# Optimization experiments

Measured on AMD Instinct MI355X. Metric: run time of the kernel, lower is better.

Reference implementation:

```python
import jax, jax.numpy as jnp
import numpy as np

LOSS_IDX = jnp.array([0, 1])    # loss_indices from __init__
BASIS_IDX = jnp.array([0, 1])   # dtw_mapping_basis (x, y)


def _dtw_path(cost):
    """Classic DTW DP + backtrack on cost [N, M].
    Returns padded alignment path (a, b) of length N+M-1 with validity mask.
    DP is run as an anti-diagonal wavefront scan (L = N+M-1 steps)."""
    N, M = cost.shape
    L = N + M - 1
    inf = jnp.float32(jnp.inf)
    i_idx = jnp.arange(N)

    def diag_step(carry, k):
        prev1, prev2 = carry  # diagonals k-1 and k-2, indexed by row i
        j = k - i_idx
        valid = (j >= 0) & (j < M)
        c = cost[i_idx, jnp.clip(j, 0, M - 1)]
        up = jnp.concatenate([jnp.full((1,), inf), prev1[:-1]])  # D[i-1, j]
        dg = jnp.concatenate([jnp.full((1,), inf), prev2[:-1]])  # D[i-1, j-1]
        lf = prev1                                               # D[i, j-1]
        best = jnp.minimum(jnp.minimum(up, dg), lf)
        best = jnp.where(jnp.isinf(best), jnp.float32(0.0), best)  # (0,0) seed
        cur = jnp.where(valid, c + best, inf)
        return (cur, prev1), cur

    init = (jnp.full((N,), inf), jnp.full((N,), inf))
    _, diags = jax.lax.scan(diag_step, init, jnp.arange(L))  # [L, N]: D[i,j] = diags[i+j, i]

    def getD(i, j):
        ok = (i >= 0) & (j >= 0)
        return jnp.where(ok, diags[jnp.clip(i + j, 0, L - 1), jnp.clip(i, 0, N - 1)], inf)

    def bt_step(carry, _):
        i, j, done = carry
        emit_valid = jnp.logical_not(done)
        cand = jnp.stack([getD(i - 1, j - 1), getD(i - 1, j), getD(i, j - 1)])
        m = jnp.argmin(cand)  # 0: diag, 1: up, 2: left
        ni = jnp.where(m == 2, i, i - 1)
        nj = jnp.where(m == 1, j, j - 1)
        done2 = done | ((i == 0) & (j == 0))
        ni = jnp.where(done2, 0, ni)
        nj = jnp.where(done2, 0, nj)
        return (ni, nj, done2), (i, j, emit_valid)

    init_bt = (jnp.int32(N - 1), jnp.int32(M - 1), jnp.bool_(False))
    _, (a, b, valid) = jax.lax.scan(bt_step, init_bt, None, length=L)
    return a, b, valid


def _dtw_loss_single(pred, targ, subcoef):
    # DTW alignment is computed on detached (numpy in torch) basis coords.
    p = jax.lax.stop_gradient(pred)[:, BASIS_IDX]
    t = jax.lax.stop_gradient(targ)[:, BASIS_IDX]
    # euclidean pairwise distance cost [N, M]
    cost = jnp.sqrt(jnp.sum((p[:, None, :] - t[None, :, :]) ** 2, axis=-1))
    a, b, valid = _dtw_path(cost)
    d = jnp.abs(pred[a][:, LOSS_IDX] - targ[b][:, LOSS_IDX]) * subcoef  # [L, 2]
    return jnp.sum(d * valid[:, None].astype(d.dtype))


def setup_inputs() -> dict:
    key = jax.random.key(0)
    k1, k2 = jax.random.split(key)
    B, N, M, F = 32, 1024, 1024, 4
    preds = jax.random.normal(k1, (B, N, F), dtype=jnp.float32)
    targs = jax.random.normal(k2, (B, M, F), dtype=jnp.float32)
    subcoef = jnp.ones((2,), dtype=jnp.float32)
    return {"preds": preds, "targs": targs, "subcoef": subcoef}


def reference(preds, targs, subcoef):
    per_sample = jax.vmap(_dtw_loss_single, in_axes=(0, 0, None))(preds, targs, subcoef)
    return jnp.sum(per_sample)
```

## Files before the change

kernel.cpp:

```cpp
#include <hip/hip_runtime.h>
#include <math.h>

#define BATCH 32
#define NN 1024
#define MM 1024
#define LPATH (NN + MM - 1)

#define PB 128
#define PQ 128
#define GB 8
#define GH 8
#define PAN_WORDS 1536
#define BAT_WORDS (GB * GH * PAN_WORDS)
#define RCPL (9 * 1024)
#define RC_OFFW ((size_t)BATCH * BAT_WORDS)
#define BR_OFFW (RC_OFFW + (size_t)BATCH * RCPL)
#define WS_WORDS (BR_OFFW + (size_t)BATCH * RCPL)
#define REQ_WS_NEW (WS_WORDS * 4)

#define DEC_WORDS_PER_BATCH ((NN / 4) * (MM / 4))
#define REQ_WS ((size_t)BATCH * DEC_WORDS_PER_BATCH * 4)

__global__ void init_kernel(float* out) { out[0] = 0.0f; }

__global__ void init2(float* __restrict__ ws, float* __restrict__ out)
{
    const int b = blockIdx.x, t = threadIdx.x;
    const float INF = __builtin_inff();
    if (b == 0 && t == 0) out[0] = 0.0f;
    float* rc0 = ws + RC_OFFW + (size_t)b * RCPL;
    float* br0 = ws + BR_OFFW + (size_t)b * RCPL;
    for (int i = t; i < 1024; i += 256) { rc0[i] = INF; br0[i] = INF; }
}

__device__ __forceinline__ float wave_shr1(float v)
{
    return __int_as_float(__builtin_amdgcn_update_dpp(
        __float_as_int(v), __float_as_int(v), 0x138, 0xF, 0xF, false));
}

__global__ __launch_bounds__(64, 1) void dtw_panel(
    const float* __restrict__ preds, const float* __restrict__ targs,
    float* __restrict__ ws, const int diag)
{
    const int b = blockIdx.y;
    const int r0 = (diag > GH - 1) ? diag - (GH - 1) : 0;
    const int r = r0 + blockIdx.x;
    const int c = diag - r;
    const int l = threadIdx.x;
    const float INF = __builtin_inff();

    __shared__ __align__(16) float txP[260], tyP[260];
    __shared__ __align__(16) float TL[200];
    __shared__ __align__(16) float botL[128];

    if (l < 63) { txP[l] = 0.f; tyP[l] = 0.f; }
    txP[191 + l] = 0.f; tyP[191 + l] = 0.f;
    if (l < 6) { txP[255 + l] = 0.f; tyP[255 + l] = 0.f; }
    TL[128 + l] = INF; if (l < 8) TL[192 + l] = INF;

    const float4* tg4 = (const float4*)targs + (size_t)b * MM + c * PQ;
    {
        const float4 a = tg4[l], e = tg4[64 + l];
        txP[63 + l] = a.x;      tyP[63 + l] = a.y;
        txP[63 + 64 + l] = e.x; tyP[63 + 64 + l] = e.y;
    }
    const float* browR = ws + BR_OFFW + ((size_t)b * 9 + r) * 1024 + c * PQ;
    TL[l] = browR[l]; TL[64 + l] = browR[64 + l];

    const float4* pp4 = (const float4*)preds + (size_t)b * NN + r * PB;
    const float4 p0 = pp4[2 * l], p1 = pp4[2 * l + 1];
    const float px0 = p0.x, py0 = p0.y, px1 = p1.x, py1 = p1.y;

    const float* rc = ws + RC_OFFW + ((size_t)b * 9 + c) * 1024 + r * PB;
    float D0 = rc[2 * l], D1 = rc[2 * l + 1];
    const float corner = (c == 0) ? ((r == 0) ? 0.0f : INF) : browR[-1];
    const float dg0init = (l == 0) ? corner : rc[2 * l - 1];

    unsigned* __restrict__ decP = (unsigned*)ws + (size_t)b * BAT_WORDS
                                + (size_t)(r * GH + c) * PAN_WORDS + l;
    __syncthreads();

    float txb[8], tyb[8];
    #pragma unroll
    for (int k = 0; k < 4; ++k) { txb[k] = txP[63 + k - l]; tyb[k] = tyP[63 + k - l]; }
    float up0prev = INF;

    for (int it = 0; it < 24; ++it) {
        const int s0 = it * 8;
        const float4 T4a = *(const float4*)&TL[s0];
        const float4 T4b = *(const float4*)&TL[s0 + 4];
        const float Tv[8] = {T4a.x, T4a.y, T4a.z, T4a.w,
                             T4b.x, T4b.y, T4b.z, T4b.w};
        unsigned word = 0;
        #pragma unroll
        for (int k = 0; k < 8; ++k) {
            const int s = s0 + k;
            const int jq = s - l;
            txb[(k + 4) & 7] = txP[63 + jq + 4];
            tyb[(k + 4) & 7] = tyP[63 + jq + 4];
            const float sh = wave_shr1(D1);
            const float up0 = (l == 0) ? Tv[k] : sh;
            const float dg0 = (jq == 0) ? dg0init : up0prev;
            const float tx = txb[k], ty = tyb[k];
            const float dx0 = px0 - tx, dy0 = py0 - ty;
            const float c0 = __builtin_amdgcn_sqrtf(dx0 * dx0 + dy0 * dy0);
            const float mn0 = fminf(dg0, fminf(up0, D0));
            const float D0n = c0 + mn0;
            const unsigned m0 = (mn0 == dg0) ? 0u : ((mn0 == up0) ? 1u : 2u);
            const float dg1 = D0;
            const float dx1 = px1 - tx, dy1 = py1 - ty;
            const float c1 = __builtin_amdgcn_sqrtf(dx1 * dx1 + dy1 * dy1);
            const float mn1 = fminf(dg1, fminf(D0n, D1));
            const float D1n = c1 + mn1;
            const unsigned m1 = (mn1 == dg1) ? 0u : ((mn1 == D0n) ? 1u : 2u);
            word |= (m0 | (m1 << 2)) << (4 * k);
            const bool act = (jq >= 0) && (jq < PQ);
            if (act) { D0 = D0n; D1 = D1n; }
            up0prev = up0;
            if (l == 63 && act) botL[jq] = D1n;
        }
        decP[it * 64] = word;
    }

    float* rcw = ws + RC_OFFW + ((size_t)b * 9 + (c + 1)) * 1024 + r * PB;
    rcw[2 * l] = D0; rcw[2 * l + 1] = D1;
    __syncthreads();
    float* brw = ws + BR_OFFW + ((size_t)b * 9 + (r + 1)) * 1024 + c * PQ;
    brw[l] = botL[l]; brw[64 + l] = botL[64 + l];
}

__global__ __launch_bounds__(256, 1) void dtw_bt(
    const float* __restrict__ preds, const float* __restrict__ targs,
    const float* __restrict__ subcoef, const float* __restrict__ ws,
    float* __restrict__ out)
{
    const int b = blockIdx.x, t = threadIdx.x;
    __shared__ float pxA[NN], pyA[NN], txA[MM], tyA[MM];
    __shared__ unsigned path[2048];
    __shared__ int sN;
    __shared__ float wsum[4];

    for (int it = 0; it < 4; ++it) {
        const int idx = it * 256 + t;
        const float4 p4 = ((const float4*)preds)[(size_t)b * NN + idx];
        pxA[idx] = p4.x; pyA[idx] = p4.y;
        const float4 t4 = ((const float4*)targs)[(size_t)b * MM + idx];
        txA[idx] = t4.x; tyA[idx] = t4.y;
    }
    __syncthreads();

    if (t == 0) {
        const unsigned* __restrict__ decB =
            (const unsigned*)ws + (size_t)b * BAT_WORDS;
        int i = NN - 1, j = MM - 1, n = 0;
        int cwidx = -1; unsigned cw = 0;
        while (true) {
            path[n++] = ((unsigned)i << 16) | (unsigned)j;
            if ((i | j) == 0) break;
            const int ll = (i & 127) >> 1;
            const int ss = ll + (j & 127);
            const int widx = (((i >> 7) << 3) + (j >> 7)) * PAN_WORDS
                           + (ss >> 3) * 64 + ll;
            if (widx != cwidx) { cw = decB[widx]; cwidx = widx; }
            const unsigned m = (cw >> ((ss & 7) * 4 + (i & 1) * 2)) & 3u;
            i -= (m != 2u); j -= (m != 1u);
        }
        sN = n;
    }
    __syncthreads();

    const float sc0 = subcoef[0], sc1 = subcoef[1];
    const int n = sN;
    float acc = 0.0f;
    for (int p = t; p < n; p += 256) {
        const unsigned e = path[p];
        const int i = (int)(e >> 16), j = (int)(e & 0xffffu);
        acc += fabsf(pxA[i] - txA[j]) * sc0 + fabsf(pyA[i] - tyA[j]) * sc1;
    }
    #pragma unroll
    for (int o = 32; o > 0; o >>= 1) acc += __shfl_down(acc, o);
    if ((t & 63) == 0) wsum[t >> 6] = acc;
    __syncthreads();
    if (t == 0) atomicAdd(out, (wsum[0] + wsum[1]) + (wsum[2] + wsum[3]));
}

__device__ inline void bt_walk4(const unsigned* __restrict__ sdec, int roff,
                                int iLow, int& i, int& j, int& n,
                                unsigned* __restrict__ path)
{
    int ri = i >> 2, jc = j >> 2;
    unsigned w = sdec[(ri - roff) * 256 + jc];
    while (true) {
        const int base = (ri - roff) * 256 + jc;
        const unsigned wl = sdec[(jc > 0)    ? base - 1   : base];
        const unsigned wu = sdec[(ri > roff) ? base - 256 : base];
        const unsigned wd = sdec[(ri > roff && jc > 0) ? base - 257 : base];
        bool done = false, susp = false;
        while (true) {
            path[n++] = ((unsigned)i << 16) | (unsigned)j;
            if ((i | j) == 0) { done = true; break; }
            const unsigned m = (w >> (((i & 3) * 4 + (j & 3)) * 2)) & 3u;
            i -= (m != 2u); j -= (m != 1u);
            if (i < iLow) { susp = true; break; }
            if ((i >> 2) != ri || (j >> 2) != jc) break;
        }
        if (done || susp) break;
        const int nri = i >> 2, njc = j >> 2;
        w = (nri == ri) ? wl : ((njc == jc) ? wu : wd);
        ri = nri; jc = njc;
    }
}

#define RRL 4
#define CCL 4
#define LANES 64
#define NWAVE 4
#define TPBL (MM / 4)
#define NSUP (TPBL + LANES - 1)
#define LAG 72
#define TOTL (NSUP + (NWAVE - 1) * LAG)
#define DEPTH 32

__global__ __launch_bounds__(256, 1) void dtw_fused_legacy(
    const float* __restrict__ preds, const float* __restrict__ targs,
    const float* __restrict__ subcoef, unsigned* __restrict__ dec,
    float* __restrict__ out)
{
    const int b = blockIdx.x, t = threadIdx.x;
    const int l = t & 63, w = t >> 6;
    const float INF = __builtin_inff();

    __shared__ float pxA[NN], pyA[NN], txA[MM], tyA[MM];
    __shared__ float4 ring[NWAVE - 1][DEPTH];
    __shared__ unsigned sdec[128 * 256];
    __shared__ unsigned path[LPATH + 1];
    __shared__ int sI, sJ, sN;
    __shared__ float wsum[NWAVE];

    for (int it = 0; it < NN / 256; ++it) {
        const int idx = it * 256 + t;
        const float4 p4 = ((const float4*)preds)[(size_t)b * NN + idx];
        pxA[idx] = p4.x; pyA[idx] = p4.y;
        const float4 t4 = ((const float4*)targs)[(size_t)b * MM + idx];
        txA[idx] = t4.x; tyA[idx] = t4.y;
    }
    __syncthreads();

    const int i0 = (w << 8) + (l << 2);
    const float4 px4 = ((const float4*)pxA)[i0 >> 2];
    const float4 py4 = ((const float4*)pyA)[i0 >> 2];
    const float px[RRL] = {px4.x, px4.y, px4.z, px4.w};
    const float py[RRL] = {py4.x, py4.y, py4.z, py4.w};
    unsigned* __restrict__ decW =
        dec + (size_t)b * DEC_WORDS_PER_BATCH + ((size_t)w << 14) + (size_t)l;

    float Dp[RRL], Dbot[CCL], bv[CCL];
    #pragma unroll
    for (int r = 0; r < RRL; ++r) Dp[r] = INF;
    #pragma unroll
    for (int c = 0; c < CCL; ++c) { Dbot[c] = INF; bv[c] = INF; }
    float bndRet = (w == 0 && l == 0) ? 0.0f : INF;
    float4 gcur = make_float4(INF, INF, INF, INF);
    float4 tx4 = ((const float4*)txA)[0], ty4 = ((const float4*)tyA)[0];
    const float4* __restrict__ ringR = ring[(w > 0) ? (w - 1) : 0];

    for (int u = 0; u < TOTL; ++u) {
        const int ul = u - LAG * w;
        if (l == 0) {
            const bool gb = (w > 0) && (ul >= 0) && (ul < TPBL);
            bv[0] = gb ? gcur.x : INF; bv[1] = gb ? gcur.y : INF;
            bv[2] = gb ? gcur.z : INF; bv[3] = gb ? gcur.w : INF;
        }
        const bool act = (ul >= l) && (ul < l + TPBL);
        if (act) {
            const float cx[CCL] = {tx4.x, tx4.y, tx4.z, tx4.w};
            const float cy[CCL] = {ty4.x, ty4.y, ty4.z, ty4.w};
            float cost[RRL][CCL];
            #pragma unroll
            for (int c = 0; c < CCL; ++c)
                #pragma unroll
                for (int r = 0; r < RRL; ++r) {
                    const float dx = px[r] - cx[c], dy = py[r] - cy[c];
                    cost[r][c] = __builtin_amdgcn_sqrtf(dx * dx + dy * dy);
                }
            unsigned word = 0;
            #pragma unroll
            for (int c = 0; c < CCL; ++c) {
                float up = bv[c];
                float dg = (c == 0) ? bndRet : bv[c - 1];
                #pragma unroll
                for (int r = 0; r < RRL; ++r) {
                    const float lf = Dp[r];
                    const unsigned m = (dg <= up && dg <= lf) ? 0u
                                     : ((up <= lf) ? 1u : 2u);
                    const float D = cost[r][c] + fminf(dg, fminf(up, lf));
                    word |= m << ((r * 4 + c) * 2);
                    dg = lf; up = D; Dp[r] = D;
                }
                Dbot[c] = up;
            }
            decW[(ul & 255) << 6] = word;
            if (l == LANES - 1 && w < NWAVE - 1)
                ring[w][ul & (DEPTH - 1)] =
                    make_float4(Dbot[0], Dbot[1], Dbot[2], Dbot[3]);
        }
        bndRet = bv[CCL - 1];
        #pragma unroll
        for (int c = 0; c < CCL; ++c) bv[c] = __shfl_up(Dbot[c], 1);
        const int un = ul + 1;
        if (un >= l && un < l + TPBL) {
            const int jn = CCL * (un - l);
            tx4 = ((const float4*)txA)[jn >> 2];
            ty4 = ((const float4*)tyA)[jn >> 2];
        }
        if (w > 0 && un >= 0 && un < TPBL)
            gcur = ringR[(un + 63) & (DEPTH - 1)];
        if ((u & 7) == 7) __syncthreads();
    }

    __threadfence_block();
    __syncthreads();

    const unsigned* __restrict__ decB = dec + (size_t)b * DEC_WORDS_PER_BATCH;
    {
        const uint4* g4 = (const uint4*)(decB + 32768);
        for (int k = t; k < 8192; k += 256) {
            const uint4 v = g4[k];
            const int kb = k << 2;
            const int wv = kb >> 14;
            const int rem = kb & 16383;
            const int q = rem >> 6;
            const int lb = rem & 63;
            const unsigned wd[4] = {v.x, v.y, v.z, v.w};
            #pragma unroll
            for (int e = 0; e < 4; ++e) {
                const int ll = lb + e;
                const int row = (wv << 6) + ll;
                const int jc = (q - ll) & 255;
                sdec[(row << 8) + jc] = wd[e];
            }
        }
    }
    __syncthreads();
    if (t == 0) {
        int i = NN - 1, j = MM - 1, n = 0;
        bt_walk4(sdec, 128, 512, i, j, n, path);
        sI = i; sJ = j; sN = n;
    }
    __syncthreads();
    {
        const uint4* g4 = (const uint4*)decB;
        for (int k = t; k < 8192; k += 256) {
            const uint4 v = g4[k];
            const int kb = k << 2;
            const int wv = kb >> 14;
            const int rem = kb & 16383;
            const int q = rem >> 6;
            const int lb = rem & 63;
            const unsigned wd[4] = {v.x, v.y, v.z, v.w};
            #pragma unroll
            for (int e = 0; e < 4; ++e) {
                const int ll = lb + e;
                const int row = (wv << 6) + ll;
                const int jc = (q - ll) & 255;
                sdec[(row << 8) + jc] = wd[e];
            }
        }
    }
    __syncthreads();
    if (t == 0) {
        int i = sI, j = sJ, n = sN;
        bt_walk4(sdec, 0, 0, i, j, n, path);
        sN = n;
    }
    __syncthreads();

    const float sc0 = subcoef[0], sc1 = subcoef[1];
    const int n = sN;
    float acc = 0.0f;
    for (int p = t; p < n; p += 256) {
        const unsigned e = path[p];
        const int i = (int)(e >> 16), j = (int)(e & 0xffffu);
        acc += fabsf(pxA[i] - txA[j]) * sc0 + fabsf(pyA[i] - tyA[j]) * sc1;
    }
    #pragma unroll
    for (int o = 32; o > 0; o >>= 1) acc += __shfl_down(acc, o);
    if ((t & 63) == 0) wsum[t >> 6] = acc;
    __syncthreads();
    if (t == 0) atomicAdd(out, (wsum[0] + wsum[1]) + (wsum[2] + wsum[3]));
}

__global__ __launch_bounds__(256) void dtw_fallback(
    const float* __restrict__ preds, const float* __restrict__ targs,
    const float* __restrict__ subcoef, unsigned* __restrict__ dec,
    float* __restrict__ out)
{
    const int b = blockIdx.x;
    const int t = threadIdx.x;
    const float INF = __builtin_inff();
    __shared__ float px[NN], py[NN];
    __shared__ float txy[2 * MM];
    __shared__ float bbuf[2][256];

    for (int it = 0; it < NN / 256; ++it) {
        const int idx = it * 256 + t;
        const float4 p4 = ((const float4*)preds)[(size_t)b * NN + idx];
        px[idx] = p4.x; py[idx] = p4.y;
        const float4 t4 = ((const float4*)targs)[(size_t)b * MM + idx];
        txy[2 * idx] = t4.x; txy[2 * idx + 1] = t4.y;
    }
    bbuf[0][t] = INF; bbuf[1][t] = INF;
    __syncthreads();

    float pxr[4], pyr[4], Dp[4];
    #pragma unroll
    for (int r = 0; r < 4; ++r) {
        pxr[r] = px[4 * t + r]; pyr[r] = py[4 * t + r]; Dp[r] = INF;
    }
    float dgB = (t == 0) ? 0.0f : INF;
    unsigned packed = 0;
    unsigned* decB = dec + (size_t)b * 65536;
    for (int s = 0; s < MM + 255; ++s) {
        const int j = s - t;
        const float upB = (t == 0) ? INF : bbuf[(s + 1) & 1][t - 1];
        if (j >= 0 && j < MM) {
            const float txj = txy[2 * j], tyj = txy[2 * j + 1];
            float up = upB, dg = dgB;
            unsigned mbits = 0;
            #pragma unroll
            for (int r = 0; r < 4; ++r) {
                const float dx = pxr[r] - txj, dy = pyr[r] - tyj;
                const float c = sqrtf(dx * dx + dy * dy);
                const float lf = Dp[r];
                const unsigned m = (dg <= up && dg <= lf) ? 0u
                                 : ((up <= lf) ? 1u : 2u);
                mbits |= m << (r * 8 + (j & 3) * 2);
                const float Dc = c + fminf(up, fminf(dg, lf));
                dg = lf; up = Dc; Dp[r] = Dc;
            }
            packed |= mbits;
            if ((j & 3) == 3) { decB[(unsigned)t * 256 + (j >> 2)] = packed; packed = 0; }
            bbuf[s & 1][t] = Dp[3];
        }
        dgB = upB;
        __syncthreads();
    }
    __threadfence_block();
    __syncthreads();
    if (t == 0) {
        const float sc0 = subcoef[0], sc1 = subcoef[1];
        int i = NN - 1, jj = MM - 1;
        float loss = 0.0f;
        int ti = i >> 2, tj = jj >> 2;
        unsigned wv = decB[ti * 256 + tj];
        while (true) {
            const int tjl = (tj > 0) ? tj - 1 : 0;
            const int til = (ti > 0) ? ti - 1 : 0;
            const unsigned wl = decB[ti * 256 + tjl];
            const unsigned wu = decB[til * 256 + tj];
            const unsigned wd = decB[til * 256 + tjl];
            bool done = false;
            while (true) {
                loss += fabsf(px[i] - txy[2 * jj]) * sc0
                      + fabsf(py[i] - txy[2 * jj + 1]) * sc1;
                if ((i | jj) == 0) { done = true; break; }
                const unsigned m = (wv >> (((i & 3) * 4 + (jj & 3)) * 2)) & 3u;
                i -= (m != 2u); jj -= (m != 1u);
                if ((i >> 2) != ti || (jj >> 2) != tj) break;
            }
            if (done) break;
            const int nti = i >> 2, ntj = jj >> 2;
            wv = (nti == ti) ? wl : ((ntj == tj) ? wu : wd);
            ti = nti; tj = ntj;
        }
        atomicAdd(out, loss);
    }
}

extern "C" void kernel_launch(void* const* d_in, const int* in_sizes, int n_in,
                              void* d_out, int out_size, void* d_ws, size_t ws_size,
                              hipStream_t stream) {
    const float* preds   = (const float*)d_in[0];
    const float* targs   = (const float*)d_in[1];
    const float* subcoef = (const float*)d_in[2];
    float* out = (float*)d_out;

    if (ws_size >= REQ_WS_NEW) {
        float* wsf = (float*)d_ws;
        init2<<<BATCH, 256, 0, stream>>>(wsf, out);
        for (int d = 0; d < GB + GH - 1; ++d) {
            const int r0 = (d > GH - 1) ? d - (GH - 1) : 0;
            const int r1 = (d < GB - 1) ? d : GB - 1;
            dim3 grid(r1 - r0 + 1, BATCH);
            dtw_panel<<<grid, 64, 0, stream>>>(preds, targs, wsf, d);
        }
        dtw_bt<<<BATCH, 256, 0, stream>>>(preds, targs, subcoef, wsf, out);
    } else if (ws_size >= REQ_WS) {
        unsigned* dec = (unsigned*)d_ws;
        init_kernel<<<1, 1, 0, stream>>>(out);
        dtw_fused_legacy<<<BATCH, 256, 0, stream>>>(preds, targs, subcoef, dec, out);
    } else {
        unsigned* dec = (unsigned*)d_ws;
        init_kernel<<<1, 1, 0, stream>>>(out);
        dtw_fallback<<<BATCH, 256, 0, stream>>>(preds, targs, subcoef, dec, out);
    }
}
```

Before: 540.3 us.

## Replace per-diagonal panel launches with persistent row-band kernel using flag handoff

Fifteen per-anti-diagonal kernel launches are replaced by one persistent kernel with 256 blocks, one per (batch, row band). Each block sweeps its eight column panels in order and keeps the right-edge DP state in registers instead of round-tripping it through global memory. Before each panel it spin-waits on an acquire flag for the bottom row written by the band above. This is meant to remove launch gaps and per-panel global traffic. It relies on all blocks being co-resident to avoid deadlock, and it adds a redundant duplicate targets load loop.

```diff
diff --git a/kernel.cpp b/kernel.cpp
--- a/kernel.cpp
+++ b/kernel.cpp
@@ -12,10 +12,11 @@
 #define GH 8
 #define PAN_WORDS 1536
 #define BAT_WORDS (GB * GH * PAN_WORDS)
-#define RCPL (9 * 1024)
-#define RC_OFFW ((size_t)BATCH * BAT_WORDS)
-#define BR_OFFW (RC_OFFW + (size_t)BATCH * RCPL)
-#define WS_WORDS (BR_OFFW + (size_t)BATCH * RCPL)
+#define DEC_WORDS ((size_t)BATCH * BAT_WORDS)
+#define BR_OFFW DEC_WORDS
+#define BRPL (9 * 1024)
+#define FL_OFFW (BR_OFFW + (size_t)BATCH * BRPL)
+#define WS_WORDS (FL_OFFW + (size_t)BATCH * 64)
 #define REQ_WS_NEW (WS_WORDS * 4)
 
 #define DEC_WORDS_PER_BATCH ((NN / 4) * (MM / 4))
@@ -23,14 +24,11 @@
 
 __global__ void init_kernel(float* out) { out[0] = 0.0f; }
 
-__global__ void init2(float* __restrict__ ws, float* __restrict__ out)
-{
-    const int b = blockIdx.x, t = threadIdx.x;
-    const float INF = __builtin_inff();
-    if (b == 0 && t == 0) out[0] = 0.0f;
-    float* rc0 = ws + RC_OFFW + (size_t)b * RCPL;
-    float* br0 = ws + BR_OFFW + (size_t)b * RCPL;
-    for (int i = t; i < 1024; i += 256) { rc0[i] = INF; br0[i] = INF; }
+__global__ void init3(unsigned* __restrict__ wsu, float* __restrict__ out)
+{
+    const int t = threadIdx.x;
+    if (t == 0) out[0] = 0.0f;
+    for (int i = t; i < BATCH * 64; i += 256) wsu[FL_OFFW + i] = 0u;
 }
 
 __device__ __forceinline__ float wave_shr1(float v)
@@ -39,95 +37,135 @@
         __float_as_int(v), __float_as_int(v), 0x138, 0xF, 0xF, false));
 }
 
-__global__ __launch_bounds__(64, 1) void dtw_panel(
+__global__ __launch_bounds__(64, 1) void dtw_dp(
     const float* __restrict__ preds, const float* __restrict__ targs,
-    float* __restrict__ ws, const int diag)
-{
-    const int b = blockIdx.y;
-    const int r0 = (diag > GH - 1) ? diag - (GH - 1) : 0;
-    const int r = r0 + blockIdx.x;
-    const int c = diag - r;
+    unsigned* __restrict__ wsu)
+{
+    const int blk = blockIdx.x;
+    const int b = blk >> 3, r = blk & 7;
     const int l = threadIdx.x;
     const float INF = __builtin_inff();
 
-    __shared__ __align__(16) float txP[260], tyP[260];
-    __shared__ __align__(16) float TL[200];
+    __shared__ __align__(16) float txA[1160], tyA[1160];
+    __shared__ __align__(16) float TL[208];
     __shared__ __align__(16) float botL[128];
 
-    if (l < 63) { txP[l] = 0.f; tyP[l] = 0.f; }
-    txP[191 + l] = 0.f; tyP[191 + l] = 0.f;
-    if (l < 6) { txP[255 + l] = 0.f; tyP[255 + l] = 0.f; }
-    TL[128 + l] = INF; if (l < 8) TL[192 + l] = INF;
-
-    const float4* tg4 = (const float4*)targs + (size_t)b * MM + c * PQ;
+    for (int i = l; i < 64; i += 64) { txA[i] = 0.f; tyA[i] = 0.f; }
+    for (int i = 1087 + l; i < 1160; i += 64) { txA[i] = 0.f; tyA[i] = 0.f; }
+    if (l < 16) TL[192 + l] = INF;
+    TL[128 + l] = INF;
+    if (r == 0) { TL[l] = INF; TL[64 + l] = INF; }
+
     {
-        const float4 a = tg4[l], e = tg4[64 + l];
-        txP[63 + l] = a.x;      tyP[63 + l] = a.y;
-        txP[63 + 64 + l] = e.x; tyP[63 + 64 + l] = e.y;
-    }
-    const float* browR = ws + BR_OFFW + ((size_t)b * 9 + r) * 1024 + c * PQ;
-    TL[l] = browR[l]; TL[64 + l] = browR[64 + l];
+        const float4* tg4 = (const float4*)targs + (size_t)b * MM;
+        #pragma unroll
+        for (int k = 0; k < 4; ++k) {
+            const float4 v = tg4[k * 64 + l];
+            const int j = 63 + 4 * (k * 64 + l);
+            txA[j] = v.x; tyA[j] = v.y;
+            const float4 w = tg4[k * 64 + l];
+            (void)w;
+        }
+    }
+    {
+        const float4* tg4 = (const float4*)targs + (size_t)b * MM;
+        for (int j = l; j < MM; j += 64) {
+            const float4 v = tg4[j];
+            txA[63 + j] = v.x; tyA[63 + j] = v.y;
+        }
+    }
 
     const float4* pp4 = (const float4*)preds + (size_t)b * NN + r * PB;
     const float4 p0 = pp4[2 * l], p1 = pp4[2 * l + 1];
     const float px0 = p0.x, py0 = p0.y, px1 = p1.x, py1 = p1.y;
 
-    const float* rc = ws + RC_OFFW + ((size_t)b * 9 + c) * 1024 + r * PB;
-    float D0 = rc[2 * l], D1 = rc[2 * l + 1];
-    const float corner = (c == 0) ? ((r == 0) ? 0.0f : INF) : browR[-1];
-    const float dg0init = (l == 0) ? corner : rc[2 * l - 1];
-
-    unsigned* __restrict__ decP = (unsigned*)ws + (size_t)b * BAT_WORDS
-                                + (size_t)(r * GH + c) * PAN_WORDS + l;
-    __syncthreads();
-
-    float txb[8], tyb[8];
-    #pragma unroll
-    for (int k = 0; k < 4; ++k) { txb[k] = txP[63 + k - l]; tyb[k] = tyP[63 + k - l]; }
-    float up0prev = INF;
-
-    for (int it = 0; it < 24; ++it) {
-        const int s0 = it * 8;
-        const float4 T4a = *(const float4*)&TL[s0];
-        const float4 T4b = *(const float4*)&TL[s0 + 4];
-        const float Tv[8] = {T4a.x, T4a.y, T4a.z, T4a.w,
-                             T4b.x, T4b.y, T4b.z, T4b.w};
-        unsigned word = 0;
+    unsigned* __restrict__ browI = wsu + BR_OFFW + (size_t)b * BRPL;
+    unsigned* __restrict__ flagB = wsu + FL_OFFW + (size_t)b * 64;
+
+    float D0 = INF, D1 = INF;
+    __syncthreads();
+
+    for (int c = 0; c < GH; ++c) {
+        float tlm1;
+        if (r > 0) {
+            const int fi = (r - 1) * 8 + c;
+            while (__hip_atomic_load(&flagB[fi], __ATOMIC_ACQUIRE,
+                                     __HIP_MEMORY_SCOPE_AGENT) == 0u)
+                __builtin_amdgcn_s_sleep(1);
+            const unsigned* bp = browI + (size_t)r * 1024 + c * PQ;
+            TL[2 * l] = __int_as_float(__hip_atomic_load(
+                (unsigned*)&bp[2 * l], __ATOMIC_RELAXED, __HIP_MEMORY_SCOPE_AGENT));
+            TL[2 * l + 1] = __int_as_float(__hip_atomic_load(
+                (unsigned*)&bp[2 * l + 1], __ATOMIC_RELAXED, __HIP_MEMORY_SCOPE_AGENT));
+            tlm1 = (c == 0) ? INF
+                 : __int_as_float(__hip_atomic_load((unsigned*)&bp[-1],
+                       __ATOMIC_RELAXED, __HIP_MEMORY_SCOPE_AGENT));
+        } else {
+            tlm1 = (c == 0) ? 0.0f : INF;
+        }
+        const float sh1 = wave_shr1(D1);
+        const float dg0init = (l == 0) ? tlm1 : ((c == 0) ? INF : sh1);
+
+        unsigned* __restrict__ decP = wsu + (size_t)b * BAT_WORDS
+                                    + (size_t)(r * GH + c) * PAN_WORDS + l;
+        const int cb = 63 + c * PQ;
+
+        float txb[8], tyb[8];
         #pragma unroll
-        for (int k = 0; k < 8; ++k) {
-            const int s = s0 + k;
-            const int jq = s - l;
-            txb[(k + 4) & 7] = txP[63 + jq + 4];
-            tyb[(k + 4) & 7] = tyP[63 + jq + 4];
-            const float sh = wave_shr1(D1);
-            const float up0 = (l == 0) ? Tv[k] : sh;
-            const float dg0 = (jq == 0) ? dg0init : up0prev;
-            const float tx = txb[k], ty = tyb[k];
-            const float dx0 = px0 - tx, dy0 = py0 - ty;
-            const float c0 = __builtin_amdgcn_sqrtf(dx0 * dx0 + dy0 * dy0);
-            const float mn0 = fminf(dg0, fminf(up0, D0));
-            const float D0n = c0 + mn0;
-            const unsigned m0 = (mn0 == dg0) ? 0u : ((mn0 == up0) ? 1u : 2u);
-            const float dg1 = D0;
-            const float dx1 = px1 - tx, dy1 = py1 - ty;
-            const float c1 = __builtin_amdgcn_sqrtf(dx1 * dx1 + dy1 * dy1);
-            const float mn1 = fminf(dg1, fminf(D0n, D1));
-            const float D1n = c1 + mn1;
-            const unsigned m1 = (mn1 == dg1) ? 0u : ((mn1 == D0n) ? 1u : 2u);
-            word |= (m0 | (m1 << 2)) << (4 * k);
-            const bool act = (jq >= 0) && (jq < PQ);
-            if (act) { D0 = D0n; D1 = D1n; }
-            up0prev = up0;
-            if (l == 63 && act) botL[jq] = D1n;
-        }
-        decP[it * 64] = word;
-    }
-
-    float* rcw = ws + RC_OFFW + ((size_t)b * 9 + (c + 1)) * 1024 + r * PB;
-    rcw[2 * l] = D0; rcw[2 * l + 1] = D1;
-    __syncthreads();
-    float* brw = ws + BR_OFFW + ((size_t)b * 9 + (r + 1)) * 1024 + c * PQ;
-    brw[l] = botL[l]; brw[64 + l] = botL[64 + l];
+        for (int k = 0; k < 4; ++k) {
+            txb[k] = txA[cb + k - l]; tyb[k] = tyA[cb + k - l];
+        }
+        float up0prev = INF;
+
+        for (int it = 0; it < 24; ++it) {
+            const int s0 = it * 8;
+            const float4 T4a = *(const float4*)&TL[s0];
+            const float4 T4b = *(const float4*)&TL[s0 + 4];
+            const float Tv[8] = {T4a.x, T4a.y, T4a.z, T4a.w,
+                                 T4b.x, T4b.y, T4b.z, T4b.w};
+            unsigned word = 0;
+            #pragma unroll
+            for (int k = 0; k < 8; ++k) {
+                const int s = s0 + k;
+                const int jq = s - l;
+                txb[(k + 4) & 7] = txA[cb + jq + 4];
+                tyb[(k + 4) & 7] = tyA[cb + jq + 4];
+                const float sh = wave_shr1(D1);
+                const float up0 = (l == 0) ? Tv[k] : sh;
+                const float dg0 = (jq == 0) ? dg0init : up0prev;
+                const float tx = txb[k], ty = tyb[k];
+                const float dx0 = px0 - tx, dy0 = py0 - ty;
+                const float c0 = __builtin_amdgcn_sqrtf(dx0 * dx0 + dy0 * dy0);
+                const float mn0 = fminf(dg0, fminf(up0, D0));
+                const float D0n = c0 + mn0;
+                const unsigned m0 = (mn0 == dg0) ? 0u : ((mn0 == up0) ? 1u : 2u);
+                const float dg1 = D0;
+                const float dx1 = px1 - tx, dy1 = py1 - ty;
+                const float c1 = __builtin_amdgcn_sqrtf(dx1 * dx1 + dy1 * dy1);
+                const float mn1 = fminf(dg1, fminf(D0n, D1));
+                const float D1n = c1 + mn1;
+                const unsigned m1 = (mn1 == dg1) ? 0u : ((mn1 == D0n) ? 1u : 2u);
+                word |= (m0 | (m1 << 2)) << (4 * k);
+                const bool act = (jq >= 0) && (jq < PQ);
+                if (act) { D0 = D0n; D1 = D1n; }
+                up0prev = up0;
+                if (l == 63 && act) botL[jq] = D1n;
+            }
+            decP[it * 64] = word;
+        }
+
+        if (r < GB - 1) {
+            unsigned* bw = browI + (size_t)(r + 1) * 1024 + c * PQ;
+            __hip_atomic_store(&bw[2 * l], __float_as_int(botL[2 * l]),
+                               __ATOMIC_RELAXED, __HIP_MEMORY_SCOPE_AGENT);
+            __hip_atomic_store(&bw[2 * l + 1], __float_as_int(botL[2 * l + 1]),
+                               __ATOMIC_RELAXED, __HIP_MEMORY_SCOPE_AGENT);
+            __threadfence();
+            if (l == 0)
+                __hip_atomic_store(&flagB[r * 8 + c], 1u, __ATOMIC_RELEASE,
+                                   __HIP_MEMORY_SCOPE_AGENT);
+        }
+    }
 }
 
 __global__ __launch_bounds__(256, 1) void dtw_bt(
@@ -487,15 +525,11 @@
     float* out = (float*)d_out;
 
     if (ws_size >= REQ_WS_NEW) {
-        float* wsf = (float*)d_ws;
-        init2<<<BATCH, 256, 0, stream>>>(wsf, out);
-        for (int d = 0; d < GB + GH - 1; ++d) {
-            const int r0 = (d > GH - 1) ? d - (GH - 1) : 0;
-            const int r1 = (d < GB - 1) ? d : GB - 1;
-            dim3 grid(r1 - r0 + 1, BATCH);
-            dtw_panel<<<grid, 64, 0, stream>>>(preds, targs, wsf, d);
-        }
-        dtw_bt<<<BATCH, 256, 0, stream>>>(preds, targs, subcoef, wsf, out);
+        unsigned* wsu = (unsigned*)d_ws;
+        init3<<<1, 256, 0, stream>>>(wsu, out);
+        dtw_dp<<<BATCH * GB, 64, 0, stream>>>(preds, targs, wsu);
+        dtw_bt<<<BATCH, 256, 0, stream>>>(preds, targs, subcoef,
+                                          (const float*)d_ws, out);
     } else if (ws_size >= REQ_WS) {
         unsigned* dec = (unsigned*)d_ws;
         init_kernel<<<1, 1, 0, stream>>>(out);
```

After: 625.6 us. 1.16x slower.

## Stage backtrack decision bands in LDS with double-buffered prefetch

Applied to the files above, without the earlier changes.

The backtrack kernel now walks the DTW path one 128-row band at a time, reading 2-bit decisions from shared memory instead of chasing global memory with a single thread. While thread 0 walks the current band, the other 255 threads copy the next band from the workspace into a second LDS buffer, hiding global load latency behind the serial walk. This adds about 96KB of LDS per block and a barrier per band, and it copies whole bands even where the path touches only part of one.

```diff
diff --git a/kernel.cpp b/kernel.cpp
--- a/kernel.cpp
+++ b/kernel.cpp
@@ -12,6 +12,7 @@
 #define GH 8
 #define PAN_WORDS 1536
 #define BAT_WORDS (GB * GH * PAN_WORDS)
+#define BAND_W (GH * PAN_WORDS)
 #define RCPL (9 * 1024)
 #define RC_OFFW ((size_t)BATCH * BAT_WORDS)
 #define BR_OFFW (RC_OFFW + (size_t)BATCH * RCPL)
@@ -132,13 +133,14 @@
 
 __global__ __launch_bounds__(256, 1) void dtw_bt(
     const float* __restrict__ preds, const float* __restrict__ targs,
-    const float* __restrict__ subcoef, const float* __restrict__ ws,
+    const float* __restrict__ subcoef, const unsigned* __restrict__ wsu,
     float* __restrict__ out)
 {
     const int b = blockIdx.x, t = threadIdx.x;
     __shared__ float pxA[NN], pyA[NN], txA[MM], tyA[MM];
+    __shared__ __align__(16) unsigned sbuf[2][BAND_W];
     __shared__ unsigned path[2048];
-    __shared__ int sN;
+    __shared__ int sI, sJ, sN;
     __shared__ float wsum[4];
 
     for (int it = 0; it < 4; ++it) {
@@ -148,27 +150,43 @@
         const float4 t4 = ((const float4*)targs)[(size_t)b * MM + idx];
         txA[idx] = t4.x; tyA[idx] = t4.y;
     }
-    __syncthreads();
-
-    if (t == 0) {
-        const unsigned* __restrict__ decB =
-            (const unsigned*)ws + (size_t)b * BAT_WORDS;
-        int i = NN - 1, j = MM - 1, n = 0;
-        int cwidx = -1; unsigned cw = 0;
-        while (true) {
-            path[n++] = ((unsigned)i << 16) | (unsigned)j;
-            if ((i | j) == 0) break;
-            const int ll = (i & 127) >> 1;
-            const int ss = ll + (j & 127);
-            const int widx = (((i >> 7) << 3) + (j >> 7)) * PAN_WORDS
-                           + (ss >> 3) * 64 + ll;
-            if (widx != cwidx) { cw = decB[widx]; cwidx = widx; }
-            const unsigned m = (cw >> ((ss & 7) * 4 + (i & 1) * 2)) & 3u;
-            i -= (m != 2u); j -= (m != 1u);
-        }
-        sN = n;
-    }
-    __syncthreads();
+    const unsigned* __restrict__ decB = wsu + (size_t)b * BAT_WORDS;
+
+    {
+        uint4* d4 = (uint4*)sbuf[7 & 1];
+        const uint4* s4 = (const uint4*)(decB + (size_t)7 * BAND_W);
+        for (int k = t; k < BAND_W / 4; k += 256) d4[k] = s4[k];
+    }
+    if (t == 0) { sI = NN - 1; sJ = MM - 1; sN = 0; }
+    __syncthreads();
+
+    for (int r = 7; r >= 0; --r) {
+        if (t == 0) {
+            int i = sI, j = sJ, n = sN;
+            if (i >= 0) {
+                const unsigned* __restrict__ sd = sbuf[r & 1];
+                const int iLow = r << 7;
+                int cwidx = -1; unsigned cw = 0;
+                while (true) {
+                    path[n++] = ((unsigned)i << 16) | (unsigned)j;
+                    if ((i | j) == 0) { i = -1; break; }
+                    const int ll = (i & 127) >> 1;
+                    const int ss = ll + (j & 127);
+                    const int widx = (j >> 7) * PAN_WORDS + (ss >> 3) * 64 + ll;
+                    if (widx != cwidx) { cw = sd[widx]; cwidx = widx; }
+                    const unsigned m = (cw >> ((ss & 7) * 4 + (i & 1) * 2)) & 3u;
+                    i -= (m != 2u); j -= (m != 1u);
+                    if (i < iLow) break;
+                }
+            }
+            sI = i; sJ = j; sN = n;
+        } else if (r > 0) {
+            uint4* d4 = (uint4*)sbuf[(r - 1) & 1];
+            const uint4* s4 = (const uint4*)(decB + (size_t)(r - 1) * BAND_W);
+            for (int k = t - 1; k < BAND_W / 4; k += 255) d4[k] = s4[k];
+        }
+        __syncthreads();
+    }
 
     const float sc0 = subcoef[0], sc1 = subcoef[1];
     const int n = sN;
@@ -495,7 +513,8 @@
             dim3 grid(r1 - r0 + 1, BATCH);
             dtw_panel<<<grid, 64, 0, stream>>>(preds, targs, wsf, d);
         }
-        dtw_bt<<<BATCH, 256, 0, stream>>>(preds, targs, subcoef, wsf, out);
+        dtw_bt<<<BATCH, 256, 0, stream>>>(preds, targs, subcoef,
+                                          (const unsigned*)d_ws, out);
     } else if (ws_size >= REQ_WS) {
         unsigned* dec = (unsigned*)d_ws;
         init_kernel<<<1, 1, 0, stream>>>(out);
```

New measurement: 562.5 us. 1.04x slower.

## Give each lane four DTW rows per panel, halving the row-panel count

Applied to the files above, without the earlier changes.

Each 64-lane panel now covers 256 rows (four per lane) instead of 128, so the grid is 4x8 panels rather than 8x8. The anti-diagonal launch sequence drops from 15 to 11 kernels, and each lane does more sequential DP work per cross-lane shift. Decision bits are repacked as two words per eight-column step, and the backtrack indexing is updated to match. The trade-off is a longer serial chain per panel step and fewer panels in flight per diagonal.

```diff
diff --git a/kernel.cpp b/kernel.cpp
--- a/kernel.cpp
+++ b/kernel.cpp
@@ -6,11 +6,11 @@
 #define MM 1024
 #define LPATH (NN + MM - 1)
 
-#define PB 128
 #define PQ 128
-#define GB 8
+#define PBR 256
+#define GB 4
 #define GH 8
-#define PAN_WORDS 1536
+#define PAN_WORDS 3072
 #define BAT_WORDS (GB * GH * PAN_WORDS)
 #define RCPL (9 * 1024)
 #define RC_OFFW ((size_t)BATCH * BAT_WORDS)
@@ -39,7 +39,7 @@
         __float_as_int(v), __float_as_int(v), 0x138, 0xF, 0xF, false));
 }
 
-__global__ __launch_bounds__(64, 1) void dtw_panel(
+__global__ __launch_bounds__(64, 1) void dtw_panel4(
     const float* __restrict__ preds, const float* __restrict__ targs,
     float* __restrict__ ws, const int diag)
 {
@@ -68,14 +68,17 @@
     const float* browR = ws + BR_OFFW + ((size_t)b * 9 + r) * 1024 + c * PQ;
     TL[l] = browR[l]; TL[64 + l] = browR[64 + l];
 
-    const float4* pp4 = (const float4*)preds + (size_t)b * NN + r * PB;
-    const float4 p0 = pp4[2 * l], p1 = pp4[2 * l + 1];
+    const float4* pp4 = (const float4*)preds + (size_t)b * NN + r * PBR;
+    const float4 p0 = pp4[4 * l],     p1 = pp4[4 * l + 1];
+    const float4 p2 = pp4[4 * l + 2], p3 = pp4[4 * l + 3];
     const float px0 = p0.x, py0 = p0.y, px1 = p1.x, py1 = p1.y;
-
-    const float* rc = ws + RC_OFFW + ((size_t)b * 9 + c) * 1024 + r * PB;
-    float D0 = rc[2 * l], D1 = rc[2 * l + 1];
+    const float px2 = p2.x, py2 = p2.y, px3 = p3.x, py3 = p3.y;
+
+    const float* rc = ws + RC_OFFW + ((size_t)b * 9 + c) * 1024 + r * PBR;
+    float D0 = rc[4 * l], D1 = rc[4 * l + 1];
+    float D2 = rc[4 * l + 2], D3 = rc[4 * l + 3];
     const float corner = (c == 0) ? ((r == 0) ? 0.0f : INF) : browR[-1];
-    const float dg0init = (l == 0) ? corner : rc[2 * l - 1];
+    const float dg0init = (l == 0) ? corner : rc[4 * l - 1];
 
     unsigned* __restrict__ decP = (unsigned*)ws + (size_t)b * BAT_WORDS
                                 + (size_t)(r * GH + c) * PAN_WORDS + l;
@@ -92,47 +95,75 @@
         const float4 T4b = *(const float4*)&TL[s0 + 4];
         const float Tv[8] = {T4a.x, T4a.y, T4a.z, T4a.w,
                              T4b.x, T4b.y, T4b.z, T4b.w};
-        unsigned word = 0;
+        unsigned w0 = 0, w1 = 0;
         #pragma unroll
         for (int k = 0; k < 8; ++k) {
             const int s = s0 + k;
             const int jq = s - l;
             txb[(k + 4) & 7] = txP[63 + jq + 4];
             tyb[(k + 4) & 7] = tyP[63 + jq + 4];
-            const float sh = wave_shr1(D1);
+            const float sh = wave_shr1(D3);
             const float up0 = (l == 0) ? Tv[k] : sh;
-            const float dg0 = (jq == 0) ? dg0init : up0prev;
             const float tx = txb[k], ty = tyb[k];
-            const float dx0 = px0 - tx, dy0 = py0 - ty;
-            const float c0 = __builtin_amdgcn_sqrtf(dx0 * dx0 + dy0 * dy0);
-            const float mn0 = fminf(dg0, fminf(up0, D0));
-            const float D0n = c0 + mn0;
-            const unsigned m0 = (mn0 == dg0) ? 0u : ((mn0 == up0) ? 1u : 2u);
-            const float dg1 = D0;
-            const float dx1 = px1 - tx, dy1 = py1 - ty;
-            const float c1 = __builtin_amdgcn_sqrtf(dx1 * dx1 + dy1 * dy1);
-            const float mn1 = fminf(dg1, fminf(D0n, D1));
-            const float D1n = c1 + mn1;
-            const unsigned m1 = (mn1 == dg1) ? 0u : ((mn1 == D0n) ? 1u : 2u);
-            word |= (m0 | (m1 << 2)) << (4 * k);
-            const bool act = (jq >= 0) && (jq < PQ);
-            if (act) { D0 = D0n; D1 = D1n; }
+            float dg = (jq == 0) ? dg0init : up0prev;
+            float up = up0;
+            unsigned mb = 0;
+            {
+                const float dx = px0 - tx, dy = py0 - ty;
+                const float cc = __builtin_amdgcn_sqrtf(dx * dx + dy * dy);
+                const float mn = fminf(dg, fminf(up, D0));
+                const float Dn = cc + mn;
+                mb |= ((mn == dg) ? 0u : ((mn == up) ? 1u : 2u)) << 0;
+                dg = D0; up = Dn; D0 = (jq >= 0 && jq < PQ) ? Dn : D0;
+                if (!(jq >= 0 && jq < PQ)) {  }
+                (void)0;
+            }
+            {
+                const float dx = px1 - tx, dy = py1 - ty;
+                const float cc = __builtin_amdgcn_sqrtf(dx * dx + dy * dy);
+                const float mn = fminf(dg, fminf(up, D1));
+                const float Dn = cc + mn;
+                mb |= ((mn == dg) ? 0u : ((mn == up) ? 1u : 2u)) << 2;
+                dg = D1; up = Dn; D1 = (jq >= 0 && jq < PQ) ? Dn : D1;
+            }
+            {
+                const float dx = px2 - tx, dy = py2 - ty;
+                const float cc = __builtin_amdgcn_sqrtf(dx * dx + dy * dy);
+                const float mn = fminf(dg, fminf(up, D2));
+                const float Dn = cc + mn;
+                mb |= ((mn == dg) ? 0u : ((mn == up) ? 1u : 2u)) << 4;
+                dg = D2; up = Dn; D2 = (jq >= 0 && jq < PQ) ? Dn : D2;
+            }
+            {
+                const float dx = px3 - tx, dy = py3 - ty;
+                const float cc = __builtin_amdgcn_sqrtf(dx * dx + dy * dy);
+                const float mn = fminf(dg, fminf(up, D3));
+                const float Dn = cc + mn;
+                mb |= ((mn == dg) ? 0u : ((mn == up) ? 1u : 2u)) << 6;
+                const bool act = (jq >= 0) && (jq < PQ);
+                if (act) { D3 = Dn; if (l == 63) botL[jq] = Dn; }
+            }
             up0prev = up0;
-            if (l == 63 && act) botL[jq] = D1n;
-        }
-        decP[it * 64] = word;
-    }
-
-    float* rcw = ws + RC_OFFW + ((size_t)b * 9 + (c + 1)) * 1024 + r * PB;
-    rcw[2 * l] = D0; rcw[2 * l + 1] = D1;
-    __syncthreads();
-    float* brw = ws + BR_OFFW + ((size_t)b * 9 + (r + 1)) * 1024 + c * PQ;
-    brw[l] = botL[l]; brw[64 + l] = botL[64 + l];
+            if (k < 4) w0 |= mb << (8 * (s & 3));
+            else       w1 |= mb << (8 * (s & 3));
+        }
+        decP[(2 * it) * 64] = w0;
+        decP[(2 * it + 1) * 64] = w1;
+    }
+
+    float* rcw = ws + RC_OFFW + ((size_t)b * 9 + (c + 1)) * 1024 + r * PBR;
+    rcw[4 * l] = D0; rcw[4 * l + 1] = D1;
+    rcw[4 * l + 2] = D2; rcw[4 * l + 3] = D3;
+    __syncthreads();
+    if (r < GB - 1) {
+        float* brw = ws + BR_OFFW + ((size_t)b * 9 + (r + 1)) * 1024 + c * PQ;
+        brw[l] = botL[l]; brw[64 + l] = botL[64 + l];
+    }
 }
 
 __global__ __launch_bounds__(256, 1) void dtw_bt(
     const float* __restrict__ preds, const float* __restrict__ targs,
-    const float* __restrict__ subcoef, const float* __restrict__ ws,
+    const float* __restrict__ subcoef, const unsigned* __restrict__ wsu,
     float* __restrict__ out)
 {
     const int b = blockIdx.x, t = threadIdx.x;
@@ -151,19 +182,18 @@
     __syncthreads();
 
     if (t == 0) {
-        const unsigned* __restrict__ decB =
-            (const unsigned*)ws + (size_t)b * BAT_WORDS;
+        const unsigned* __restrict__ decB = wsu + (size_t)b * BAT_WORDS;
         int i = NN - 1, j = MM - 1, n = 0;
         int cwidx = -1; unsigned cw = 0;
         while (true) {
             path[n++] = ((unsigned)i << 16) | (unsigned)j;
             if ((i | j) == 0) break;
-            const int ll = (i & 127) >> 1;
-            const int ss = ll + (j & 127);
-            const int widx = (((i >> 7) << 3) + (j >> 7)) * PAN_WORDS
-                           + (ss >> 3) * 64 + ll;
+            const int ll = (i & 255) >> 2;
+            const int s = (j & 127) + ll;
+            const int widx = (((i >> 8) << 3) + (j >> 7)) * PAN_WORDS
+                           + (s >> 2) * 64 + ll;
             if (widx != cwidx) { cw = decB[widx]; cwidx = widx; }
-            const unsigned m = (cw >> ((ss & 7) * 4 + (i & 1) * 2)) & 3u;
+            const unsigned m = (cw >> ((s & 3) * 8 + (i & 3) * 2)) & 3u;
             i -= (m != 2u); j -= (m != 1u);
         }
         sN = n;
@@ -493,9 +523,10 @@
             const int r0 = (d > GH - 1) ? d - (GH - 1) : 0;
             const int r1 = (d < GB - 1) ? d : GB - 1;
             dim3 grid(r1 - r0 + 1, BATCH);
-            dtw_panel<<<grid, 64, 0, stream>>>(preds, targs, wsf, d);
-        }
-        dtw_bt<<<BATCH, 256, 0, stream>>>(preds, targs, subcoef, wsf, out);
+            dtw_panel4<<<grid, 64, 0, stream>>>(preds, targs, wsf, d);
+        }
+        dtw_bt<<<BATCH, 256, 0, stream>>>(preds, targs, subcoef,
+                                          (const unsigned*)d_ws, out);
     } else if (ws_size >= REQ_WS) {
         unsigned* dec = (unsigned*)d_ws;
         init_kernel<<<1, 1, 0, stream>>>(out);
```

Result: slower. 575.9 us (+6.6%).
